# Performance work log

Hardware: AMD Instinct MI355X
Metric: run time of the kernel (lower is better)

The kernel has to match this reference:

```python
import jax, jax.numpy as jnp
import numpy as np

N = 100_000      # nodes
E = 1_600_000    # edges (avg degree 16)
DIN = 128
DOUT = 128
NEG_SLOPE = 0.2  # DGL GATConv default negative_slope


def setup_inputs() -> dict:
    key = jax.random.key(0)
    k1, k2, k3, k4, k5, k6 = jax.random.split(key, 6)
    h = jax.random.normal(k1, (N, DIN), dtype=jnp.float32)
    src = jax.random.randint(k2, (E,), 0, N, dtype=jnp.int32)
    dst = jax.random.randint(k3, (E,), 0, N, dtype=jnp.int32)
    W = jax.random.normal(k4, (DIN, DOUT), dtype=jnp.float32) / np.sqrt(DIN).astype(np.float32)
    attn_l = jax.random.normal(k5, (DOUT,), dtype=jnp.float32) * 0.1
    attn_r = jax.random.normal(k6, (DOUT,), dtype=jnp.float32) * 0.1
    return {"h": h, "src": src, "dst": dst, "W": W, "attn_l": attn_l, "attn_r": attn_r}


def reference(h, src, dst, W, attn_l, attn_r):
    # Single-head DGL GATConv (bias=False, no feat/attn dropout, no activation).
    feat = h @ W                                   # [N, D] projected features
    el = feat @ attn_l                             # [N] source attention logits
    er = feat @ attn_r                             # [N] destination attention logits
    e = jax.nn.leaky_relu(el[src] + er[dst], NEG_SLOPE)   # [E] edge scores

    # Numerically stable edge softmax, grouped by destination node.
    m = jax.ops.segment_max(e, dst, num_segments=N)        # [N]
    m = jnp.where(jnp.isfinite(m), m, 0.0)                 # nodes with no in-edges
    ex = jnp.exp(e - m[dst])                               # [E]
    denom = jax.ops.segment_sum(ex, dst, num_segments=N)   # [N]
    alpha = ex / jnp.maximum(denom[dst], jnp.float32(1e-9))  # [E]

    # Weighted aggregation of source features into destination nodes.
    out = jax.ops.segment_sum(alpha[:, None] * feat[src], dst, num_segments=N)  # [N, D]
    return out
```

## Files before the change

### kernel.cpp

```cpp
#include <hip/hip_runtime.h>
#include <hip/hip_bf16.h>

#define N_NODES 100000
#define N_EDGES 1600000
#define D 128
#define NEG_SLOPE 0.2f

#define NBKT 782
#define CAPB 4096
#define BCHUNK 8192
#define BIN_BLOCKS 196
#define GEMM_BLOCKS 782
#define CAP 2816

typedef __attribute__((ext_vector_type(8))) short s8v;
typedef __attribute__((ext_vector_type(4))) float f4v;

static __device__ __forceinline__ unsigned short f2bf(float f) {
    __hip_bfloat16 b = __float2bfloat16(f);
    return *(unsigned short*)&b;
}

__global__ __launch_bounds__(256) void wcast(
    const float* __restrict__ W, const float* __restrict__ attn_l,
    const float* __restrict__ attn_r, unsigned short* __restrict__ Wt)
{
    __shared__ float Wl[128 * 132];
    __shared__ float all[128], arl[128];
    const int t = threadIdx.x;
    for (int i = 0; i < 64; ++i) {
        const int id = t + 256 * i;
        Wl[(id >> 7) * 132 + (id & 127)] = W[id];
    }
    if (t < 128) { all[t] = attn_l[t]; arl[t] = attn_r[t]; }
    __syncthreads();
    for (int i = 0; i < 64; ++i) {
        const int id = t + 256 * i;
        const int n = id >> 7, k = id & 127;
        Wt[n * 128 + k] = f2bf(Wl[k * 132 + n]);
    }
    if (t < 128) {
        float sl = 0.f, sr = 0.f;
        for (int n = 0; n < 128; ++n) {
            const float v = Wl[t * 132 + n];
            sl += v * all[n]; sr += v * arl[n];
        }
        Wt[128 * 128 + t] = f2bf(sl);
        Wt[129 * 128 + t] = f2bf(sr);
    }
}

__global__ __launch_bounds__(512) void gemm_bin(
    const float* __restrict__ h, const unsigned short* __restrict__ Wt,
    unsigned short* __restrict__ featb, float* __restrict__ el, float* __restrict__ er,
    const int* __restrict__ src, const int* __restrict__ dst,
    int* __restrict__ gwp, unsigned int* __restrict__ eb)
{
    __shared__ __align__(16) char smem[69632];
    const int t = threadIdx.x;

    if (blockIdx.x < BIN_BLOCKS) {
        int* cnt_l            = (int*)smem;
        int* tmp              = (int*)(smem + 3128);
        int* lbase            = (int*)(smem + 7224);
        int* gbase            = (int*)(smem + 10356);
        unsigned int* slocal  = (unsigned int*)(smem + 13484);
        unsigned short* sbkt  = (unsigned short*)(smem + 46252);

        const int base = (int)blockIdx.x * BCHUNK;
        const int nloc = min(BCHUNK, N_EDGES - base);

        for (int i = t; i < NBKT; i += 512) cnt_l[i] = 0;
        __syncthreads();

        unsigned int ent[16];
        unsigned short bk[16];
#pragma unroll
        for (int j = 0; j < 16; ++j) {
            const int i = t + 512 * j;
            if (i < nloc) {
                const int s = src[base + i];
                const int d = dst[base + i];
                bk[j]  = (unsigned short)(d >> 7);
                ent[j] = (unsigned int)s | ((unsigned int)(d & 127) << 17);
                atomicAdd(&cnt_l[bk[j]], 1);
            } else bk[j] = 0xffff;
        }
        __syncthreads();

        tmp[t]       = (t < NBKT) ? cnt_l[t] : 0;
        tmp[t + 512] = (t + 512 < NBKT) ? cnt_l[t + 512] : 0;
        __syncthreads();
        for (int o = 1; o < 1024; o <<= 1) {
            const int a  = (t >= o) ? tmp[t - o] : 0;
            const int b2 = (t + 512 >= o) ? tmp[t + 512 - o] : 0;
            __syncthreads();
            tmp[t] += a; tmp[t + 512] += b2;
            __syncthreads();
        }
        for (int i = t; i < NBKT; i += 512) lbase[i] = (i == 0) ? 0 : tmp[i - 1];
        if (t == 0) lbase[NBKT] = tmp[NBKT - 1];
        __syncthreads();

        for (int b = t; b < NBKT; b += 512) {
            const int c = lbase[b + 1] - lbase[b];
            if (c) gbase[b] = b * CAPB + atomicAdd(&gwp[b], c);
            cnt_l[b] = 0;
        }
        __syncthreads();

#pragma unroll
        for (int j = 0; j < 16; ++j) {
            if (bk[j] != 0xffff) {
                const int p = lbase[bk[j]] + atomicAdd(&cnt_l[bk[j]], 1);
                slocal[p] = ent[j];
                sbkt[p]   = bk[j];
            }
        }
        __syncthreads();

        for (int i = t; i < nloc; i += 512) {
            const int b = sbkt[i];
            eb[gbase[b] + (i - lbase[b])] = slocal[i];
        }
    } else {
        unsigned short* Asmem = (unsigned short*)smem;
        unsigned short* Bsmem = (unsigned short*)(smem + 32768);

        const int w    = t >> 6;
        const int lane = t & 63;
        const int g4   = lane >> 4;
        const int cl   = lane & 15;
        const int row0 = ((int)blockIdx.x - BIN_BLOCKS) * 128;

#pragma unroll
        for (int i = 0; i < 4; ++i) {
            const int ch = t + 512 * i;
            const int r = ch >> 4, c = ch & 15;
            const int srow = min(row0 + r, N_NODES - 1);
            const float4 a = *(const float4*)&h[srow * D + c * 8];
            const float4 b = *(const float4*)&h[srow * D + c * 8 + 4];
            s8v v;
            v[0] = (short)f2bf(a.x); v[1] = (short)f2bf(a.y);
            v[2] = (short)f2bf(a.z); v[3] = (short)f2bf(a.w);
            v[4] = (short)f2bf(b.x); v[5] = (short)f2bf(b.y);
            v[6] = (short)f2bf(b.z); v[7] = (short)f2bf(b.w);
            *(s8v*)&Asmem[r * 128 + ((c ^ (r & 15)) << 3)] = v;
        }
        for (int ch = t; ch < 2080; ch += 512) {
            const int n = ch >> 4, c = ch & 15;
            *(s8v*)&Bsmem[n * 128 + ((c ^ (n & 15)) << 3)] =
                *(const s8v*)&Wt[n * 128 + c * 8];
        }
        __syncthreads();

        f4v acc[9] = {};
#pragma unroll
        for (int ks = 0; ks < 4; ++ks) {
            const int c = ks * 4 + g4;
            s8v bfr[9];
#pragma unroll
            for (int nt = 0; nt < 9; ++nt) {
                const int n = nt * 16 + cl;
                bfr[nt] = *(const s8v*)&Bsmem[n * 128 + ((c ^ cl) << 3)];
            }
            const int r = w * 16 + cl;
            const s8v af = *(const s8v*)&Asmem[r * 128 + ((c ^ cl) << 3)];
#pragma unroll
            for (int nt = 0; nt < 9; ++nt)
                acc[nt] = __builtin_amdgcn_mfma_f32_16x16x32_bf16(
                    af, bfr[nt], acc[nt], 0, 0, 0);
        }

        unsigned short* ftile = Asmem;
#pragma unroll
        for (int nt = 0; nt < 8; ++nt) {
            const int ch = 2 * nt + (cl >> 3);
#pragma unroll
            for (int reg = 0; reg < 4; ++reg) {
                const int r = w * 16 + 4 * g4 + reg;
                ftile[r * 128 + ((ch ^ (r & 15)) << 3) + (cl & 7)] =
                    f2bf(acc[nt][reg]);
            }
        }
        if (cl < 2) {
            float* dstp = (cl == 0) ? el : er;
#pragma unroll
            for (int reg = 0; reg < 4; ++reg) {
                const int rg = row0 + w * 16 + 4 * g4 + reg;
                if (rg < N_NODES) dstp[rg] = acc[8][reg];
            }
        }
        __syncthreads();
#pragma unroll
        for (int i = 0; i < 4; ++i) {
            const int ch = t + 512 * i;
            const int r = ch >> 4, c = ch & 15;
            if (row0 + r < N_NODES)
                *(s8v*)&featb[(row0 + r) * 128 + c * 8] =
                    *(const s8v*)&ftile[r * 128 + ((c ^ (r & 15)) << 3)];
        }
    }
}

__global__ __launch_bounds__(512) void aggregate(
    const int* __restrict__ gwp, const unsigned int* __restrict__ eb,
    const float* __restrict__ el, const float* __restrict__ er,
    const uint2* __restrict__ featb2, float* __restrict__ out)
{
    __shared__ __align__(8) uint2 sw[CAP];
    __shared__ int off_l[129];
    __shared__ int cnt_l[128];
    __shared__ float nsum[128];
    __shared__ float er_l[128];

    const int t = threadIdx.x;
    const int b = blockIdx.x;
    const int ne   = gwp[b];
    const int gbeg = b * CAPB;
    const int node0 = b << 7;
    const int w    = t >> 6;
    const int lane = t & 63;
    const int ll   = lane & 31;
    const int half = lane >> 5;

    if (t < 128) {
        const int nd = node0 + t;
        er_l[t] = (nd < N_NODES) ? er[nd] : 0.f;
        cnt_l[t] = 0;
        nsum[t] = 0.f;
    }
    __syncthreads();

    if (ne <= CAP) {
        unsigned int ent[6];
#pragma unroll
        for (int j = 0; j < 6; ++j) {
            const int i = t + 512 * j;
            if (i < ne) {
                ent[j] = eb[gbeg + i];
                atomicAdd(&cnt_l[(ent[j] >> 17) & 127], 1);
            }
        }
        __syncthreads();
        if (w == 0) {
            const int a  = cnt_l[2 * lane];
            const int b2 = cnt_l[2 * lane + 1];
            int inc = a + b2;
#pragma unroll
            for (int o = 1; o < 64; o <<= 1) {
                const int u = __shfl_up(inc, o, 64);
                if (lane >= o) inc += u;
            }
            const int excl = inc - (a + b2);
            off_l[2 * lane]     = excl;
            off_l[2 * lane + 1] = excl + a;
            if (lane == 63) off_l[128] = inc;
            cnt_l[2 * lane] = 0; cnt_l[2 * lane + 1] = 0;
        }
        __syncthreads();
#pragma unroll
        for (int j = 0; j < 6; ++j) {
            const int i = t + 512 * j;
            if (i < ne) {
                const unsigned int e = ent[j];
                const int dl = (e >> 17) & 127;
                const int sj = (int)(e & 0x1FFFFu);
                float sc = el[sj] + er_l[dl];
                sc = (sc > 0.f) ? sc : NEG_SLOPE * sc;
                const float ex = __expf(sc);
                const int p = off_l[dl] + atomicAdd(&cnt_l[dl], 1);
                sw[p] = make_uint2(e, __float_as_uint(ex));
                atomicAdd(&nsum[dl], ex);
            }
        }
        __syncthreads();

        for (int dl = w; dl < 128; dl += 8) {
            const int node = node0 + dl;
            if (node >= N_NODES) break;
            const int beg = off_l[dl];
            const int n   = off_l[dl + 1] - beg;
            float4 acc = make_float4(0.f, 0.f, 0.f, 0.f);
            const int iters = (n + 1) >> 1;
            for (int tt = 0; tt < iters; ++tt) {
                const int idx = 2 * tt + half;
                const uint2 p = sw[beg + min(idx, n - 1)];
                const float wj = (idx < n) ? __uint_as_float(p.y) : 0.f;
                const int  sjj = (int)(p.x & 0x1FFFFu);
                const uint2 fb = featb2[sjj * 32 + ll];
                acc.x += wj * __uint_as_float(fb.x << 16);
                acc.y += wj * __uint_as_float(fb.x & 0xffff0000u);
                acc.z += wj * __uint_as_float(fb.y << 16);
                acc.w += wj * __uint_as_float(fb.y & 0xffff0000u);
            }
            acc.x += __shfl_xor(acc.x, 32, 64);
            acc.y += __shfl_xor(acc.y, 32, 64);
            acc.z += __shfl_xor(acc.z, 32, 64);
            acc.w += __shfl_xor(acc.w, 32, 64);
            const float rs = 1.f / fmaxf(nsum[dl], 1e-9f);
            if (lane < 32)
                *(float4*)&out[node * D + ll * 4] =
                    make_float4(acc.x * rs, acc.y * rs, acc.z * rs, acc.w * rs);
        }
    } else {
        for (int dl = w; dl < 128; dl += 8) {
            const int node = node0 + dl;
            if (node >= N_NODES) break;
            float4 acc = make_float4(0.f, 0.f, 0.f, 0.f);
            float ssum = 0.f;
            for (int ch = 0; ch < ne; ch += 64) {
                const int nn = min(64, ne - ch);
                float ex = 0.f; int sj = 0;
                if (lane < nn) {
                    const unsigned int e = eb[gbeg + ch + lane];
                    if ((int)((e >> 17) & 127) == dl) {
                        sj = (int)(e & 0x1FFFFu);
                        float sc = el[sj] + er_l[dl];
                        sc = (sc > 0.f) ? sc : NEG_SLOPE * sc;
                        ex = __expf(sc);
                    }
                }
                ssum += ex;
                const int iters = (nn + 1) >> 1;
                for (int tt = 0; tt < iters; ++tt) {
                    const int idx = 2 * tt + half;
                    const float wj = __shfl(ex, idx, 64);
                    const int  sjj = __shfl(sj, idx, 64);
                    if (wj > 0.f) {
                        const uint2 fb = featb2[sjj * 32 + ll];
                        acc.x += wj * __uint_as_float(fb.x << 16);
                        acc.y += wj * __uint_as_float(fb.x & 0xffff0000u);
                        acc.z += wj * __uint_as_float(fb.y << 16);
                        acc.w += wj * __uint_as_float(fb.y & 0xffff0000u);
                    }
                }
            }
#pragma unroll
            for (int o = 1; o < 64; o <<= 1) ssum += __shfl_xor(ssum, o, 64);
            acc.x += __shfl_xor(acc.x, 32, 64);
            acc.y += __shfl_xor(acc.y, 32, 64);
            acc.z += __shfl_xor(acc.z, 32, 64);
            acc.w += __shfl_xor(acc.w, 32, 64);
            const float rs = 1.f / fmaxf(ssum, 1e-9f);
            if (lane < 32)
                *(float4*)&out[node * D + ll * 4] =
                    make_float4(acc.x * rs, acc.y * rs, acc.z * rs, acc.w * rs);
        }
    }
}

extern "C" void kernel_launch(void* const* d_in, const int* in_sizes, int n_in,
                              void* d_out, int out_size, void* d_ws, size_t ws_size,
                              hipStream_t stream)
{
    const float* h      = (const float*)d_in[0];
    const int*   src    = (const int*)  d_in[1];
    const int*   dst    = (const int*)  d_in[2];
    const float* W      = (const float*)d_in[3];
    const float* attn_l = (const float*)d_in[4];
    const float* attn_r = (const float*)d_in[5];
    float* out = (float*)d_out;

    char* ws = (char*)d_ws;
    unsigned short* featb = (unsigned short*)ws; ws += (size_t)N_NODES * D * 2;
    unsigned short* Wt    = (unsigned short*)ws; ws += (size_t)130 * 128 * 2;
    ws = (char*)(((size_t)ws + 15) & ~(size_t)15);
    float* el  = (float*)ws; ws += (size_t)N_NODES * sizeof(float);
    float* er  = (float*)ws; ws += (size_t)N_NODES * sizeof(float);
    int*   gwp = (int*)ws;   ws += (size_t)NBKT * sizeof(int);
    ws = (char*)(((size_t)ws + 15) & ~(size_t)15);
    unsigned int* eb = (unsigned int*)ws; ws += (size_t)NBKT * CAPB * sizeof(unsigned int);

    hipMemsetAsync(gwp, 0, (size_t)NBKT * sizeof(int), stream);

    wcast<<<1, 256, 0, stream>>>(W, attn_l, attn_r, Wt);
    gemm_bin<<<BIN_BLOCKS + GEMM_BLOCKS, 512, 0, stream>>>(
        h, Wt, featb, el, er, src, dst, gwp, eb);
    aggregate<<<NBKT, 512, 0, stream>>>(gwp, eb, el, er, (const uint2*)featb, out);
}
```

Before: 206.2 us.

## Shrink gemm_bin LDS, stream A from global, widen aggregate gathers to 16B

The binning phase now uses half-size chunks with twice as many blocks, and the GEMM reads h rows straight into MFMA A-fragments instead of staging them in LDS. Together these cut the shared-memory footprint of gemm_bin so more blocks can be resident. In the aggregate fast path, each lane gathers 16-byte feature chunks and handles 8 edges per iteration across four lane-quads, giving more loads in flight, at the cost of an extra shuffle reduction stage. The GEMM gains an extra barrier before reusing Bsmem as the output tile, and its per-lane A loads from global may coalesce less well than the old staged copy.

```diff
diff --git a/kernel.cpp b/kernel.cpp
--- a/kernel.cpp
+++ b/kernel.cpp
@@ -8,8 +8,8 @@
 
 #define NBKT 782
 #define CAPB 4096
-#define BCHUNK 8192
-#define BIN_BLOCKS 196
+#define BCHUNK 4096
+#define BIN_BLOCKS 391
 #define GEMM_BLOCKS 782
 #define CAP 2816
 
@@ -19,6 +19,12 @@
 static __device__ __forceinline__ unsigned short f2bf(float f) {
     __hip_bfloat16 b = __float2bfloat16(f);
     return *(unsigned short*)&b;
+}
+static __device__ __forceinline__ float bflo(unsigned int u) {
+    return __uint_as_float(u << 16);
+}
+static __device__ __forceinline__ float bfhi(unsigned int u) {
+    return __uint_as_float(u & 0xffff0000u);
 }
 
 __global__ __launch_bounds__(256) void wcast(
@@ -56,16 +62,16 @@
     const int* __restrict__ src, const int* __restrict__ dst,
     int* __restrict__ gwp, unsigned int* __restrict__ eb)
 {
-    __shared__ __align__(16) char smem[69632];
+    __shared__ __align__(16) char smem[38144];
     const int t = threadIdx.x;
 
     if (blockIdx.x < BIN_BLOCKS) {
         int* cnt_l            = (int*)smem;
-        int* tmp              = (int*)(smem + 3128);
-        int* lbase            = (int*)(smem + 7224);
-        int* gbase            = (int*)(smem + 10356);
-        unsigned int* slocal  = (unsigned int*)(smem + 13484);
-        unsigned short* sbkt  = (unsigned short*)(smem + 46252);
+        int* lbase            = (int*)(smem + 3136);
+        int* gbase            = (int*)(smem + 6272);
+        int* tmp              = (int*)(smem + 9408);
+        unsigned int* slocal  = (unsigned int*)(smem + 13504);
+        unsigned short* sbkt  = (unsigned short*)(smem + 29888);
 
         const int base = (int)blockIdx.x * BCHUNK;
         const int nloc = min(BCHUNK, N_EDGES - base);
@@ -73,10 +79,10 @@
         for (int i = t; i < NBKT; i += 512) cnt_l[i] = 0;
         __syncthreads();
 
-        unsigned int ent[16];
-        unsigned short bk[16];
-#pragma unroll
-        for (int j = 0; j < 16; ++j) {
+        unsigned int ent[8];
+        unsigned short bk[8];
+#pragma unroll
+        for (int j = 0; j < 8; ++j) {
             const int i = t + 512 * j;
             if (i < nloc) {
                 const int s = src[base + i];
@@ -110,7 +116,7 @@
         __syncthreads();
 
 #pragma unroll
-        for (int j = 0; j < 16; ++j) {
+        for (int j = 0; j < 8; ++j) {
             if (bk[j] != 0xffff) {
                 const int p = lbase[bk[j]] + atomicAdd(&cnt_l[bk[j]], 1);
                 slocal[p] = ent[j];
@@ -124,29 +130,15 @@
             eb[gbase[b] + (i - lbase[b])] = slocal[i];
         }
     } else {
-        unsigned short* Asmem = (unsigned short*)smem;
-        unsigned short* Bsmem = (unsigned short*)(smem + 32768);
+        unsigned short* Bsmem = (unsigned short*)smem;
 
         const int w    = t >> 6;
         const int lane = t & 63;
         const int g4   = lane >> 4;
         const int cl   = lane & 15;
         const int row0 = ((int)blockIdx.x - BIN_BLOCKS) * 128;
-
-#pragma unroll
-        for (int i = 0; i < 4; ++i) {
-            const int ch = t + 512 * i;
-            const int r = ch >> 4, c = ch & 15;
-            const int srow = min(row0 + r, N_NODES - 1);
-            const float4 a = *(const float4*)&h[srow * D + c * 8];
-            const float4 b = *(const float4*)&h[srow * D + c * 8 + 4];
-            s8v v;
-            v[0] = (short)f2bf(a.x); v[1] = (short)f2bf(a.y);
-            v[2] = (short)f2bf(a.z); v[3] = (short)f2bf(a.w);
-            v[4] = (short)f2bf(b.x); v[5] = (short)f2bf(b.y);
-            v[6] = (short)f2bf(b.z); v[7] = (short)f2bf(b.w);
-            *(s8v*)&Asmem[r * 128 + ((c ^ (r & 15)) << 3)] = v;
-        }
+        const int arow = min(row0 + w * 16 + cl, N_NODES - 1);
+
         for (int ch = t; ch < 2080; ch += 512) {
             const int n = ch >> 4, c = ch & 15;
             *(s8v*)&Bsmem[n * 128 + ((c ^ (n & 15)) << 3)] =
@@ -158,21 +150,27 @@
 #pragma unroll
         for (int ks = 0; ks < 4; ++ks) {
             const int c = ks * 4 + g4;
+            const float4 a0 = *(const float4*)&h[arow * D + c * 8];
+            const float4 a1 = *(const float4*)&h[arow * D + c * 8 + 4];
+            s8v af;
+            af[0] = (short)f2bf(a0.x); af[1] = (short)f2bf(a0.y);
+            af[2] = (short)f2bf(a0.z); af[3] = (short)f2bf(a0.w);
+            af[4] = (short)f2bf(a1.x); af[5] = (short)f2bf(a1.y);
+            af[6] = (short)f2bf(a1.z); af[7] = (short)f2bf(a1.w);
             s8v bfr[9];
 #pragma unroll
             for (int nt = 0; nt < 9; ++nt) {
                 const int n = nt * 16 + cl;
                 bfr[nt] = *(const s8v*)&Bsmem[n * 128 + ((c ^ cl) << 3)];
             }
-            const int r = w * 16 + cl;
-            const s8v af = *(const s8v*)&Asmem[r * 128 + ((c ^ cl) << 3)];
 #pragma unroll
             for (int nt = 0; nt < 9; ++nt)
                 acc[nt] = __builtin_amdgcn_mfma_f32_16x16x32_bf16(
                     af, bfr[nt], acc[nt], 0, 0, 0);
         }
 
-        unsigned short* ftile = Asmem;
+        __syncthreads();
+        unsigned short* ftile = Bsmem;
 #pragma unroll
         for (int nt = 0; nt < 8; ++nt) {
             const int ch = 2 * nt + (cl >> 3);
@@ -206,7 +204,7 @@
 __global__ __launch_bounds__(512) void aggregate(
     const int* __restrict__ gwp, const unsigned int* __restrict__ eb,
     const float* __restrict__ el, const float* __restrict__ er,
-    const uint2* __restrict__ featb2, float* __restrict__ out)
+    const uint4* __restrict__ featb4, float* __restrict__ out)
 {
     __shared__ __align__(8) uint2 sw[CAP];
     __shared__ int off_l[129];
@@ -221,8 +219,8 @@
     const int node0 = b << 7;
     const int w    = t >> 6;
     const int lane = t & 63;
-    const int ll   = lane & 31;
-    const int half = lane >> 5;
+    const int q    = lane >> 4;
+    const int lq   = lane & 15;
 
     if (t < 128) {
         const int nd = node0 + t;
@@ -281,29 +279,49 @@
             if (node >= N_NODES) break;
             const int beg = off_l[dl];
             const int n   = off_l[dl + 1] - beg;
-            float4 acc = make_float4(0.f, 0.f, 0.f, 0.f);
-            const int iters = (n + 1) >> 1;
+            float4 accA = make_float4(0.f, 0.f, 0.f, 0.f);
+            float4 accB = make_float4(0.f, 0.f, 0.f, 0.f);
+            const int iters = (n + 7) >> 3;
             for (int tt = 0; tt < iters; ++tt) {
-                const int idx = 2 * tt + half;
-                const uint2 p = sw[beg + min(idx, n - 1)];
-                const float wj = (idx < n) ? __uint_as_float(p.y) : 0.f;
-                const int  sjj = (int)(p.x & 0x1FFFFu);
-                const uint2 fb = featb2[sjj * 32 + ll];
-                acc.x += wj * __uint_as_float(fb.x << 16);
-                acc.y += wj * __uint_as_float(fb.x & 0xffff0000u);
-                acc.z += wj * __uint_as_float(fb.y << 16);
-                acc.w += wj * __uint_as_float(fb.y & 0xffff0000u);
-            }
-            acc.x += __shfl_xor(acc.x, 32, 64);
-            acc.y += __shfl_xor(acc.y, 32, 64);
-            acc.z += __shfl_xor(acc.z, 32, 64);
-            acc.w += __shfl_xor(acc.w, 32, 64);
+                const int i0 = 8 * tt + q;
+                const int i1 = 8 * tt + 4 + q;
+                const uint2 p0 = sw[beg + min(i0, n - 1)];
+                const uint2 p1 = sw[beg + min(i1, n - 1)];
+                const float w0 = (i0 < n) ? __uint_as_float(p0.y) : 0.f;
+                const float w1 = (i1 < n) ? __uint_as_float(p1.y) : 0.f;
+                const uint4 f0 = featb4[(p0.x & 0x1FFFFu) * 16 + lq];
+                const uint4 f1 = featb4[(p1.x & 0x1FFFFu) * 16 + lq];
+                accA.x += w0 * bflo(f0.x); accA.y += w0 * bfhi(f0.x);
+                accA.z += w0 * bflo(f0.y); accA.w += w0 * bfhi(f0.y);
+                accB.x += w0 * bflo(f0.z); accB.y += w0 * bfhi(f0.z);
+                accB.z += w0 * bflo(f0.w); accB.w += w0 * bfhi(f0.w);
+                accA.x += w1 * bflo(f1.x); accA.y += w1 * bfhi(f1.x);
+                accA.z += w1 * bflo(f1.y); accA.w += w1 * bfhi(f1.y);
+                accB.x += w1 * bflo(f1.z); accB.y += w1 * bfhi(f1.z);
+                accB.z += w1 * bflo(f1.w); accB.w += w1 * bfhi(f1.w);
+            }
+#pragma unroll
+            for (int o = 16; o < 64; o <<= 1) {
+                accA.x += __shfl_xor(accA.x, o, 64);
+                accA.y += __shfl_xor(accA.y, o, 64);
+                accA.z += __shfl_xor(accA.z, o, 64);
+                accA.w += __shfl_xor(accA.w, o, 64);
+                accB.x += __shfl_xor(accB.x, o, 64);
+                accB.y += __shfl_xor(accB.y, o, 64);
+                accB.z += __shfl_xor(accB.z, o, 64);
+                accB.w += __shfl_xor(accB.w, o, 64);
+            }
             const float rs = 1.f / fmaxf(nsum[dl], 1e-9f);
-            if (lane < 32)
-                *(float4*)&out[node * D + ll * 4] =
-                    make_float4(acc.x * rs, acc.y * rs, acc.z * rs, acc.w * rs);
+            if (lane < 16) {
+                *(float4*)&out[node * D + lq * 8] =
+                    make_float4(accA.x * rs, accA.y * rs, accA.z * rs, accA.w * rs);
+                *(float4*)&out[node * D + lq * 8 + 4] =
+                    make_float4(accB.x * rs, accB.y * rs, accB.z * rs, accB.w * rs);
+            }
         }
     } else {
+        const int ll   = lane & 31;
+        const int half = lane >> 5;
         for (int dl = w; dl < 128; dl += 8) {
             const int node = node0 + dl;
             if (node >= N_NODES) break;
@@ -328,11 +346,9 @@
                     const float wj = __shfl(ex, idx, 64);
                     const int  sjj = __shfl(sj, idx, 64);
                     if (wj > 0.f) {
-                        const uint2 fb = featb2[sjj * 32 + ll];
-                        acc.x += wj * __uint_as_float(fb.x << 16);
-                        acc.y += wj * __uint_as_float(fb.x & 0xffff0000u);
-                        acc.z += wj * __uint_as_float(fb.y << 16);
-                        acc.w += wj * __uint_as_float(fb.y & 0xffff0000u);
+                        const uint2 fb = ((const uint2*)featb4)[sjj * 32 + ll];
+                        acc.x += wj * bflo(fb.x); acc.y += wj * bfhi(fb.x);
+                        acc.z += wj * bflo(fb.y); acc.w += wj * bfhi(fb.y);
                     }
                 }
             }
@@ -377,5 +393,5 @@
     wcast<<<1, 256, 0, stream>>>(W, attn_l, attn_r, Wt);
     gemm_bin<<<BIN_BLOCKS + GEMM_BLOCKS, 512, 0, stream>>>(
         h, Wt, featb, el, er, src, dst, gwp, eb);
-    aggregate<<<NBKT, 512, 0, stream>>>(gwp, eb, el, er, (const uint2*)featb, out);
-}
+    aggregate<<<NBKT, 512, 0, stream>>>(gwp, eb, el, er, (const uint4*)featb, out);
+}
```

New measurement: 216.2 us. 4.8% more time.
